# Performance work log

Hardware: AMD Instinct MI355X
Metric: run time of the kernel (lower is better)

## Reference

```python
import jax, jax.numpy as jnp
import numpy as np

N = 100000      # nodes (size_src == size_dst)
E = 1_600_000   # edges, avg degree 16
IN = 128
HID = 128
OUT = 64
DROP_P = 0.5


def setup_inputs() -> dict:
    key = jax.random.key(0)
    ks = jax.random.split(key, 10)
    x = jax.random.normal(ks[0], (N, IN), dtype=jnp.float32)
    edge = jax.random.randint(ks[1], (2, E), 0, N, dtype=jnp.int32)
    # CuGraphSAGEConv: Linear(2*in_channels -> out_channels) over concat([agg, x]), with bias
    def lin_init(k, fan_in, fan_out):
        return jax.random.normal(k, (fan_in, fan_out), dtype=jnp.float32) / np.sqrt(fan_in)
    w0 = lin_init(ks[2], 2 * IN, HID); b0 = jnp.zeros((HID,), jnp.float32)
    w1 = lin_init(ks[3], 2 * HID, HID); b1 = jnp.zeros((HID,), jnp.float32)
    w2 = lin_init(ks[4], 2 * HID, HID); b2 = jnp.zeros((HID,), jnp.float32)
    lin_w = lin_init(ks[5], HID, OUT); lin_b = jnp.zeros((OUT,), jnp.float32)
    return {"x": x, "edge": edge, "w0": w0, "b0": b0, "w1": w1, "b1": b1,
            "w2": w2, "b2": b2, "lin_w": lin_w, "lin_b": lin_b,
            "size_src": N, "size_dst": N}


def _mean_agg(h, src, dst, n):
    # mean over incoming neighbors: agg[i] = mean_{(s->i) in E} h[s]
    msg = jnp.take(h, src, axis=0)                      # [E, d]
    s = jax.ops.segment_sum(msg, dst, num_segments=n)   # [n, d]
    deg = jax.ops.segment_sum(jnp.ones((src.shape[0],), h.dtype), dst, num_segments=n)
    return s / jnp.maximum(deg, 1.0)[:, None]


def _sage_layer(h, src, dst, n_dst, w, b, drop_key):
    agg = _mean_agg(h, src, dst, h.shape[0])            # [n, d]
    z = jnp.concatenate([agg, h], axis=-1) @ w + b      # [n, out]
    z = z[:n_dst]
    z = jax.nn.relu(z)
    keep = jax.random.bernoulli(drop_key, 1.0 - DROP_P, z.shape)
    return jnp.where(keep, z / (1.0 - DROP_P), 0.0)


def reference(x, edge, w0, b0, w1, b1, w2, b2, lin_w, lin_b, size_src, size_dst):
    src, dst = edge[0], edge[1]
    dkey = jax.random.key(42)
    h = x
    for i, (w, b) in enumerate([(w0, b0), (w1, b1), (w2, b2)]):
        h = _sage_layer(h, src, dst, size_dst, w, b, jax.random.fold_in(dkey, i))
    return h @ lin_w + lin_b
```

## Files before the change

### kernel.cpp

```cpp
#include <hip/hip_runtime.h>
#include <stdint.h>

#define NN 100000
#define NE 1600000
#define NFLAT 12800000u
#define XRANGE 12500
#define XCHUNKS 782
#define GBLK 782
#define MAXDEG 64

typedef _Float16 f16;
typedef __attribute__((ext_vector_type(2))) _Float16 f16x2;
typedef __attribute__((ext_vector_type(4))) _Float16 f16x4;
typedef __attribute__((ext_vector_type(8))) _Float16 f16x8;
typedef __attribute__((ext_vector_type(4))) float f32x4;

__device__ __forceinline__ uint32_t rotl32(uint32_t x, int r) {
  return __builtin_amdgcn_alignbit(x, x, (32 - r) & 31);
}

__device__ __forceinline__ void tf2x32(uint32_t k0, uint32_t k1,
                                       uint32_t x0, uint32_t x1,
                                       uint32_t &o0, uint32_t &o1) {
  uint32_t ks2 = k0 ^ k1 ^ 0x1BD11BDAu;
#define TF_R(r) { x0 += x1; x1 = rotl32(x1, r); x1 ^= x0; }
  x0 += k0; x1 += k1;
  TF_R(13) TF_R(15) TF_R(26) TF_R(6)
  x0 += k1;  x1 += ks2 + 1u;
  TF_R(17) TF_R(29) TF_R(16) TF_R(24)
  x0 += ks2; x1 += k0 + 2u;
  TF_R(13) TF_R(15) TF_R(26) TF_R(6)
  x0 += k0;  x1 += k1 + 3u;
  TF_R(17) TF_R(29) TF_R(16) TF_R(24)
  x0 += k1;  x1 += ks2 + 4u;
  TF_R(13) TF_R(15) TF_R(26) TF_R(6)
  x0 += ks2; x1 += k0 + 5u;
#undef TF_R
  o0 = x0; o1 = x1;
}

static void tf2x32_host(uint32_t k0, uint32_t k1, uint32_t x0, uint32_t x1,
                        uint32_t *o0, uint32_t *o1) {
  uint32_t ks2 = k0 ^ k1 ^ 0x1BD11BDAu;
#define TF_R(r) { x0 += x1; x1 = (x1 << (r)) | (x1 >> (32 - (r))); x1 ^= x0; }
  x0 += k0; x1 += k1;
  TF_R(13) TF_R(15) TF_R(26) TF_R(6)
  x0 += k1;  x1 += ks2 + 1u;
  TF_R(17) TF_R(29) TF_R(16) TF_R(24)
  x0 += ks2; x1 += k0 + 2u;
  TF_R(13) TF_R(15) TF_R(26) TF_R(6)
  x0 += k0;  x1 += k1 + 3u;
  TF_R(17) TF_R(29) TF_R(16) TF_R(24)
  x0 += k1;  x1 += ks2 + 4u;
  TF_R(13) TF_R(15) TF_R(26) TF_R(6)
  x0 += ks2; x1 += k0 + 5u;
#undef TF_R
  *o0 = x0; *o1 = x1;
}

__global__ __launch_bounds__(256) void fill_xcd(const int *__restrict__ src,
                                                const int *__restrict__ dst,
                                                int *__restrict__ cursor,
                                                int *__restrict__ col2) {
  int x = blockIdx.x & 7;
  int chunk = blockIdx.x >> 3;
  int lo = x * XRANGE, hi = lo + XRANGE;
  int base = chunk * 2048 + threadIdx.x;
#pragma unroll
  for (int t = 0; t < 8; ++t) {
    int e = base + t * 256;
    if (e < NE) {
      int d = dst[e];
      if (d >= lo && d < hi) {
        int p = atomicAdd(&cursor[d], 1);
        if (p < MAXDEG) col2[d * MAXDEG + p] = src[e];
      }
    }
  }
}

__global__ __launch_bounds__(256) void cvt_x_kernel(const float *__restrict__ x,
                                                    f16 *__restrict__ xh) {
  uint32_t i = (blockIdx.x * 256 + threadIdx.x) * 4;
  float4 v = *(const float4 *)(x + i);
  f16x4 o;
  o[0] = (f16)v.x; o[1] = (f16)v.y; o[2] = (f16)v.z; o[3] = (f16)v.w;
  *(f16x4 *)(xh + i) = o;
}

__global__ __launch_bounds__(256) void cvt_w_kernel(
    const float *__restrict__ w0, const float *__restrict__ w1,
    const float *__restrict__ w2, const float *__restrict__ lw,
    f16 *__restrict__ Wk0, f16 *__restrict__ Wk1, f16 *__restrict__ Wk2,
    f16 *__restrict__ WkL) {
  int t = blockIdx.x * 256 + threadIdx.x;
  if (t < 3 * 32768) {
    int wi = t >> 15, r = t & 32767;
    int k = r >> 7, c = r & 127;
    const float *w = (wi == 0) ? w0 : ((wi == 1) ? w1 : w2);
    f16 *o = (wi == 0) ? Wk0 : ((wi == 1) ? Wk1 : Wk2);
    o[c * 256 + k] = (f16)w[r];
  } else {
    int r = t - 3 * 32768;
    int k = r >> 6, c = r & 63;
    WkL[c * 128 + k] = (f16)lw[r];
  }
}

__global__ __launch_bounds__(256) void agg_kernel(const f16 *__restrict__ h,
                                                  const int *__restrict__ deg,
                                                  const int *__restrict__ col2,
                                                  f16 *__restrict__ agg,
                                                  uint32_t *__restrict__ mrow,
                                                  uint32_t mk0, uint32_t mk1) {
  int wid = threadIdx.x >> 6;
  int lane = threadIdx.x & 63;
  int n = blockIdx.x * 4 + wid;
  if (n >= NN) return;

  {
    uint32_t j0 = (uint32_t)n * 128u + (uint32_t)lane;
    uint32_t o0, o1, p0, p1;
    tf2x32(mk0, mk1, 0u, j0, o0, o1);
    tf2x32(mk0, mk1, 0u, j0 + 64u, p0, p1);
    unsigned long long blo = __ballot((int)(o0 ^ o1) >= 0);
    unsigned long long bhi = __ballot((int)(p0 ^ p1) >= 0);
    if (lane == 0) {
      uint4 mv;
      mv.x = (uint32_t)blo; mv.y = (uint32_t)(blo >> 32);
      mv.z = (uint32_t)bhi; mv.w = (uint32_t)(bhi >> 32);
      *(uint4 *)(mrow + (size_t)n * 4) = mv;
    }
  }

  const int beg = n * MAXDEG;
  int d = min(deg[n], MAXDEG);
  const int half = lane >> 5;
  const int q = lane & 31;
  float s0 = 0.f, s1 = 0.f, s2 = 0.f, s3 = 0.f;
  int i = 0;
  for (; i + 8 <= d; i += 8) {
    int c0 = col2[beg + i + 0 + half];
    int c1 = col2[beg + i + 2 + half];
    int c2 = col2[beg + i + 4 + half];
    int c3 = col2[beg + i + 6 + half];
    f16x4 v0 = ((const f16x4 *)(h + (size_t)c0 * 128))[q];
    f16x4 v1 = ((const f16x4 *)(h + (size_t)c1 * 128))[q];
    f16x4 v2 = ((const f16x4 *)(h + (size_t)c2 * 128))[q];
    f16x4 v3 = ((const f16x4 *)(h + (size_t)c3 * 128))[q];
    s0 += (float)v0[0] + (float)v1[0] + (float)v2[0] + (float)v3[0];
    s1 += (float)v0[1] + (float)v1[1] + (float)v2[1] + (float)v3[1];
    s2 += (float)v0[2] + (float)v1[2] + (float)v2[2] + (float)v3[2];
    s3 += (float)v0[3] + (float)v1[3] + (float)v2[3] + (float)v3[3];
  }
  for (; i + 2 <= d; i += 2) {
    int c = col2[beg + i + half];
    f16x4 v = ((const f16x4 *)(h + (size_t)c * 128))[q];
    s0 += (float)v[0]; s1 += (float)v[1];
    s2 += (float)v[2]; s3 += (float)v[3];
  }
  if (i < d && half == 0) {
    int c = col2[beg + i];
    f16x4 v = ((const f16x4 *)(h + (size_t)c * 128))[q];
    s0 += (float)v[0]; s1 += (float)v[1];
    s2 += (float)v[2]; s3 += (float)v[3];
  }
  s0 += __shfl_xor(s0, 32);
  s1 += __shfl_xor(s1, 32);
  s2 += __shfl_xor(s2, 32);
  s3 += __shfl_xor(s3, 32);
  if (half == 0) {
    float inv = 1.0f / (float)max(d, 1);
    f16x4 o;
    o[0] = (f16)(s0 * inv); o[1] = (f16)(s1 * inv);
    o[2] = (f16)(s2 * inv); o[3] = (f16)(s3 * inv);
    ((f16x4 *)(agg + (size_t)n * 128))[q] = o;
  }
}

__global__ __launch_bounds__(256) void sage_gemm_f16(
    const f16 *__restrict__ agg, const f16 *__restrict__ hin,
    const f16 *__restrict__ Wk, const float *__restrict__ bias,
    const uint32_t *__restrict__ mask, f16 *__restrict__ hout) {
  const int tid = threadIdx.x;
  const int lane = tid & 63;
  const int wv = tid >> 6;
  const int blk_row0 = blockIdx.x * 128;
  const int kg = (lane >> 4) * 8;
  const int col_lo = lane & 15;

  f16x8 Bf[2][8];
#pragma unroll
  for (int t = 0; t < 2; ++t) {
    const int colb = wv * 32 + t * 16 + col_lo;
#pragma unroll
    for (int ks = 0; ks < 8; ++ks)
      Bf[t][ks] = *(const f16x8 *)(Wk + (size_t)colb * 256 + ks * 32 + kg);
  }
  const float bv0 = bias[wv * 32 + col_lo];
  const float bv1 = bias[wv * 32 + 16 + col_lo];

#pragma unroll 2
  for (int s = 0; s < 8; ++s) {
    const int row0 = blk_row0 + s * 16;
    const int ar = row0 + col_lo;
    const bool rowok = ar < NN;
    f16x8 Af[8];
#pragma unroll
    for (int ks = 0; ks < 8; ++ks) {
      const f16 *asrc = (ks < 4)
                            ? (agg + (size_t)ar * 128 + ks * 32 + kg)
                            : (hin + (size_t)ar * 128 + (ks - 4) * 32 + kg);
      Af[ks] = rowok ? *(const f16x8 *)asrc : (f16x8){};
    }
    f32x4 acc0 = {0.f, 0.f, 0.f, 0.f}, acc1 = {0.f, 0.f, 0.f, 0.f};
#pragma unroll
    for (int ks = 0; ks < 8; ++ks) {
      acc0 = __builtin_amdgcn_mfma_f32_16x16x32_f16(Af[ks], Bf[0][ks], acc0, 0, 0, 0);
      acc1 = __builtin_amdgcn_mfma_f32_16x16x32_f16(Af[ks], Bf[1][ks], acc1, 0, 0, 0);
    }
    const int rbase = row0 + (lane >> 4) * 4;
    const int c0 = wv * 32 + col_lo;
    const int c1 = c0 + 16;
#pragma unroll
    for (int r = 0; r < 4; ++r) {
      const int row = rbase + r;
      if (row < NN) {
        uint32_t mw = mask[(size_t)row * 4 + wv];
        float z0 = acc0[r] + bv0;
        float z1 = acc1[r] + bv1;
        z0 = (z0 > 0.f && ((mw >> col_lo) & 1u)) ? z0 * 2.f : 0.f;
        z1 = (z1 > 0.f && ((mw >> (16 + col_lo)) & 1u)) ? z1 * 2.f : 0.f;
        hout[(size_t)row * 128 + c0] = (f16)z0;
        hout[(size_t)row * 128 + c1] = (f16)z1;
      }
    }
  }
}

__global__ __launch_bounds__(256) void final_gemm_f16(
    const f16 *__restrict__ hin, const f16 *__restrict__ WkL,
    const float *__restrict__ bias, float *__restrict__ outp) {
  const int tid = threadIdx.x;
  const int lane = tid & 63;
  const int wv = tid >> 6;
  const int blk_row0 = blockIdx.x * 128;
  const int kg = (lane >> 4) * 8;
  const int col_lo = lane & 15;
  const int c = wv * 16 + col_lo;
  f16x8 Bf[4];
#pragma unroll
  for (int ks = 0; ks < 4; ++ks)
    Bf[ks] = *(const f16x8 *)(WkL + (size_t)c * 128 + ks * 32 + kg);
  const float bv = bias[c];
#pragma unroll 2
  for (int s = 0; s < 8; ++s) {
    const int row0 = blk_row0 + s * 16;
    const int ar = row0 + col_lo;
    const bool rowok = ar < NN;
    f32x4 acc = {0.f, 0.f, 0.f, 0.f};
#pragma unroll
    for (int ks = 0; ks < 4; ++ks) {
      f16x8 a = rowok
                    ? *(const f16x8 *)(hin + (size_t)ar * 128 + ks * 32 + kg)
                    : (f16x8){};
      acc = __builtin_amdgcn_mfma_f32_16x16x32_f16(a, Bf[ks], acc, 0, 0, 0);
    }
    const int rbase = row0 + (lane >> 4) * 4;
#pragma unroll
    for (int r = 0; r < 4; ++r) {
      const int row = rbase + r;
      if (row < NN) outp[(size_t)row * 64 + c] = acc[r] + bv;
    }
  }
}

extern "C" void kernel_launch(void *const *d_in, const int *in_sizes, int n_in,
                              void *d_out, int out_size, void *d_ws,
                              size_t ws_size, hipStream_t stream) {
  (void)in_sizes; (void)n_in; (void)out_size; (void)ws_size;
  const float *x = (const float *)d_in[0];
  const int *edge = (const int *)d_in[1];
  const int *src = edge;
  const int *dst = edge + NE;
  const float *w0 = (const float *)d_in[2];
  const float *b0 = (const float *)d_in[3];
  const float *w1 = (const float *)d_in[4];
  const float *b1 = (const float *)d_in[5];
  const float *w2 = (const float *)d_in[6];
  const float *b2 = (const float *)d_in[7];
  const float *lw = (const float *)d_in[8];
  const float *lb = (const float *)d_in[9];
  float *out = (float *)d_out;

  char *ws = (char *)d_ws;
  f16 *xh  = (f16 *)ws; ws += (size_t)NN * 128 * 2;
  f16 *h1  = (f16 *)ws; ws += (size_t)NN * 128 * 2;
  f16 *h2  = (f16 *)ws; ws += (size_t)NN * 128 * 2;
  f16 *agg = (f16 *)ws; ws += (size_t)NN * 128 * 2;
  f16 *Wk0 = (f16 *)ws; ws += 256 * 128 * 2;
  f16 *Wk1 = (f16 *)ws; ws += 256 * 128 * 2;
  f16 *Wk2 = (f16 *)ws; ws += 256 * 128 * 2;
  f16 *WkL = (f16 *)ws; ws += 128 * 64 * 2;
  int *cursor = (int *)ws; ws += (size_t)NN * 4;
  int *col2 = (int *)ws;   ws += (size_t)NN * MAXDEG * 4;
  uint32_t *m0 = (uint32_t *)ws; ws += (size_t)(NFLAT / 32) * 4;
  uint32_t *m1 = (uint32_t *)ws; ws += (size_t)(NFLAT / 32) * 4;
  uint32_t *m2 = (uint32_t *)ws; ws += (size_t)(NFLAT / 32) * 4;

  uint32_t fk[3][2];
  for (int i = 0; i < 3; ++i)
    tf2x32_host(0u, 42u, 0u, (uint32_t)i, &fk[i][0], &fk[i][1]);

  hipMemsetAsync(cursor, 0, (size_t)NN * 4, stream);
  fill_xcd<<<8 * XCHUNKS, 256, 0, stream>>>(src, dst, cursor, col2);
  cvt_x_kernel<<<NFLAT / 1024, 256, 0, stream>>>(x, xh);
  cvt_w_kernel<<<416, 256, 0, stream>>>(w0, w1, w2, lw, Wk0, Wk1, Wk2, WkL);

  agg_kernel<<<NN / 4, 256, 0, stream>>>(xh, cursor, col2, agg, m0,
                                         fk[0][0], fk[0][1]);
  sage_gemm_f16<<<GBLK, 256, 0, stream>>>(agg, xh, Wk0, b0, m0, h1);
  agg_kernel<<<NN / 4, 256, 0, stream>>>(h1, cursor, col2, agg, m1,
                                         fk[1][0], fk[1][1]);
  sage_gemm_f16<<<GBLK, 256, 0, stream>>>(agg, h1, Wk1, b1, m1, h2);
  agg_kernel<<<NN / 4, 256, 0, stream>>>(h2, cursor, col2, agg, m2,
                                         fk[2][0], fk[2][1]);
  sage_gemm_f16<<<GBLK, 256, 0, stream>>>(agg, h2, Wk2, b2, m2, xh);
  final_gemm_f16<<<GBLK, 256, 0, stream>>>(xh, WkL, lb, out);
}
```

Before: 460.5 us.

## Pre-bin edges by destination range before building per-node adjacency lists

```diff
diff --git a/kernel.cpp b/kernel.cpp
--- a/kernel.cpp
+++ b/kernel.cpp
@@ -5,9 +5,10 @@
 #define NE 1600000
 #define NFLAT 12800000u
 #define XRANGE 12500
-#define XCHUNKS 782
 #define GBLK 782
 #define MAXDEG 64
+#define BUCKCAP 204800
+#define SBLK 98
 
 typedef _Float16 f16;
 typedef __attribute__((ext_vector_type(2))) _Float16 f16x2;
@@ -58,24 +59,45 @@
   *o0 = x0; *o1 = x1;
 }
 
-__global__ __launch_bounds__(256) void fill_xcd(const int *__restrict__ src,
-                                                const int *__restrict__ dst,
-                                                int *__restrict__ cursor,
-                                                int *__restrict__ col2) {
-  int x = blockIdx.x & 7;
-  int chunk = blockIdx.x >> 3;
-  int lo = x * XRANGE, hi = lo + XRANGE;
-  int base = chunk * 2048 + threadIdx.x;
-#pragma unroll
-  for (int t = 0; t < 8; ++t) {
-    int e = base + t * 256;
-    if (e < NE) {
-      int d = dst[e];
-      if (d >= lo && d < hi) {
-        int p = atomicAdd(&cursor[d], 1);
-        if (p < MAXDEG) col2[d * MAXDEG + p] = src[e];
-      }
-    }
+__global__ __launch_bounds__(256) void bin_edges(const int *__restrict__ src,
+                                                 const int *__restrict__ dst,
+                                                 int *__restrict__ bcnt,
+                                                 int2 *__restrict__ pairs) {
+  __shared__ int lcnt[8];
+  __shared__ int lbase[8];
+  const int tid = threadIdx.x;
+  if (tid < 8) lcnt[tid] = 0;
+  __syncthreads();
+  int e = blockIdx.x * 256 + tid;
+  int d = 0, s = 0, b = 0, pos = 0;
+  bool ok = e < NE;
+  if (ok) {
+    d = dst[e];
+    s = src[e];
+    b = d / XRANGE;
+    pos = atomicAdd(&lcnt[b], 1);
+  }
+  __syncthreads();
+  if (tid < 8) lbase[tid] = atomicAdd(&bcnt[tid], lcnt[tid]);
+  __syncthreads();
+  if (ok) {
+    int idx = lbase[b] + pos;
+    if (idx < BUCKCAP) pairs[(size_t)b * BUCKCAP + idx] = make_int2(d, s);
+  }
+}
+
+__global__ __launch_bounds__(256) void scatter_fill(const int2 *__restrict__ pairs,
+                                                    const int *__restrict__ bcnt,
+                                                    int *__restrict__ cursor,
+                                                    int *__restrict__ col2) {
+  const int x = blockIdx.x & 7;
+  const int nb = blockIdx.x >> 3;
+  const int cnt = min(bcnt[x], BUCKCAP);
+  const int2 *bp = pairs + (size_t)x * BUCKCAP;
+  for (int i = nb * 256 + threadIdx.x; i < cnt; i += SBLK * 256) {
+    int2 r = bp[i];
+    int p = atomicAdd(&cursor[r.x], 1);
+    if (p < MAXDEG) col2[r.x * MAXDEG + p] = r.y;
   }
 }
 
@@ -304,6 +326,8 @@
   f16 *WkL = (f16 *)ws; ws += 128 * 64 * 2;
   int *cursor = (int *)ws; ws += (size_t)NN * 4;
   int *col2 = (int *)ws;   ws += (size_t)NN * MAXDEG * 4;
+  int *bcnt = (int *)ws;   ws += 256;
+  int2 *pairs = (int2 *)ws; ws += (size_t)8 * BUCKCAP * 8;
   uint32_t *m0 = (uint32_t *)ws; ws += (size_t)(NFLAT / 32) * 4;
   uint32_t *m1 = (uint32_t *)ws; ws += (size_t)(NFLAT / 32) * 4;
   uint32_t *m2 = (uint32_t *)ws; ws += (size_t)(NFLAT / 32) * 4;
@@ -313,7 +337,9 @@
     tf2x32_host(0u, 42u, 0u, (uint32_t)i, &fk[i][0], &fk[i][1]);
 
   hipMemsetAsync(cursor, 0, (size_t)NN * 4, stream);
-  fill_xcd<<<8 * XCHUNKS, 256, 0, stream>>>(src, dst, cursor, col2);
+  hipMemsetAsync(bcnt, 0, 256, stream);
+  bin_edges<<<(NE + 255) / 256, 256, 0, stream>>>(src, dst, bcnt, pairs);
+  scatter_fill<<<8 * SBLK, 256, 0, stream>>>(pairs, bcnt, cursor, col2);
   cvt_x_kernel<<<NFLAT / 1024, 256, 0, stream>>>(x, xh);
   cvt_w_kernel<<<416, 256, 0, stream>>>(w0, w1, w2, lw, Wk0, Wk1, Wk2, WkL);
 
```

After: 532.7 us. +15.7%, slower.

## Bin edges by destination XCD range before per-node adjacency fill

Applied to the files above, without the earlier changes.

```diff
diff --git a/kernel.cpp b/kernel.cpp
--- a/kernel.cpp
+++ b/kernel.cpp
@@ -5,9 +5,12 @@
 #define NE 1600000
 #define NFLAT 12800000u
 #define XRANGE 12500
-#define XCHUNKS 782
 #define GBLK 782
 #define MAXDEG 64
+#define SEGSHIFT 12
+#define SEGCAP 4096
+#define NSEG 64
+#define SFBLK 128
 
 typedef _Float16 f16;
 typedef __attribute__((ext_vector_type(2))) _Float16 f16x2;
@@ -58,23 +61,51 @@
   *o0 = x0; *o1 = x1;
 }
 
-__global__ __launch_bounds__(256) void fill_xcd(const int *__restrict__ src,
-                                                const int *__restrict__ dst,
-                                                int *__restrict__ cursor,
-                                                int *__restrict__ col2) {
-  int x = blockIdx.x & 7;
-  int chunk = blockIdx.x >> 3;
-  int lo = x * XRANGE, hi = lo + XRANGE;
-  int base = chunk * 2048 + threadIdx.x;
-#pragma unroll
-  for (int t = 0; t < 8; ++t) {
-    int e = base + t * 256;
-    if (e < NE) {
-      int d = dst[e];
-      if (d >= lo && d < hi) {
-        int p = atomicAdd(&cursor[d], 1);
-        if (p < MAXDEG) col2[d * MAXDEG + p] = src[e];
-      }
+__global__ __launch_bounds__(256) void bin_edges(const int *__restrict__ src,
+                                                 const int *__restrict__ dst,
+                                                 int *__restrict__ bcnt,
+                                                 int2 *__restrict__ pairs) {
+  __shared__ int wbase[4][8];
+  const int tid = threadIdx.x;
+  const int lane = tid & 63;
+  const int wv = tid >> 6;
+  const int seg = blockIdx.x & (NSEG - 1);
+  const int e = blockIdx.x * 256 + tid;
+  const int d = dst[e];
+  const int s = src[e];
+  const int b = d / XRANGE;
+  const unsigned long long lt = (1ULL << lane) - 1ULL;
+  int pos = 0, wcnt = 0;
+#pragma unroll
+  for (int bb = 0; bb < 8; ++bb) {
+    unsigned long long mk = __ballot(b == bb);
+    if (b == bb) {
+      pos = __popcll(mk & lt);
+      wcnt = __popcll(mk);
+    }
+  }
+  if (pos == 0) wbase[wv][b] = atomicAdd(&bcnt[b * NSEG + seg], wcnt);
+  __syncthreads();
+  int idx = wbase[wv][b] + pos;
+  if (idx < SEGCAP)
+    pairs[(size_t)(b * NSEG + seg) * SEGCAP + idx] = make_int2(d, s);
+}
+
+__global__ __launch_bounds__(256) void scatter_fill(const int2 *__restrict__ pairs,
+                                                    const int *__restrict__ bcnt,
+                                                    int *__restrict__ cursor,
+                                                    int *__restrict__ col2) {
+  const int x = blockIdx.x & 7;
+  const int nb = blockIdx.x >> 3;
+  const size_t base = (size_t)x * NSEG * SEGCAP;
+  for (int i = nb * 256 + threadIdx.x; i < NSEG * SEGCAP; i += SFBLK * 256) {
+    int seg = i >> SEGSHIFT;
+    int off = i & (SEGCAP - 1);
+    int cnt = bcnt[x * NSEG + seg];
+    if (off < min(cnt, SEGCAP)) {
+      int2 r = pairs[base + i];
+      int p = atomicAdd(&cursor[r.x], 1);
+      if (p < MAXDEG) col2[r.x * MAXDEG + p] = r.y;
     }
   }
 }
@@ -304,6 +335,8 @@
   f16 *WkL = (f16 *)ws; ws += 128 * 64 * 2;
   int *cursor = (int *)ws; ws += (size_t)NN * 4;
   int *col2 = (int *)ws;   ws += (size_t)NN * MAXDEG * 4;
+  int *bcnt = (int *)ws;   ws += 8 * NSEG * 4;
+  int2 *pairs = (int2 *)ws; ws += (size_t)8 * NSEG * SEGCAP * 8;
   uint32_t *m0 = (uint32_t *)ws; ws += (size_t)(NFLAT / 32) * 4;
   uint32_t *m1 = (uint32_t *)ws; ws += (size_t)(NFLAT / 32) * 4;
   uint32_t *m2 = (uint32_t *)ws; ws += (size_t)(NFLAT / 32) * 4;
@@ -313,7 +346,9 @@
     tf2x32_host(0u, 42u, 0u, (uint32_t)i, &fk[i][0], &fk[i][1]);
 
   hipMemsetAsync(cursor, 0, (size_t)NN * 4, stream);
-  fill_xcd<<<8 * XCHUNKS, 256, 0, stream>>>(src, dst, cursor, col2);
+  hipMemsetAsync(bcnt, 0, 8 * NSEG * 4, stream);
+  bin_edges<<<NE / 256, 256, 0, stream>>>(src, dst, bcnt, pairs);
+  scatter_fill<<<8 * SFBLK, 256, 0, stream>>>(pairs, bcnt, cursor, col2);
   cvt_x_kernel<<<NFLAT / 1024, 256, 0, stream>>>(x, xh);
   cvt_w_kernel<<<416, 256, 0, stream>>>(w0, w1, w2, lw, Wk0, Wk1, Wk2, WkL);
 
```

Result: slower. 575.3 us (+24.9%).
